# Kernel tuning notes

Measured on AMD Instinct MI355X. Metric: run time of the kernel, lower is better.

Reference implementation:

```python
import jax, jax.numpy as jnp
import numpy as np

N, E, D, DOUT = 2048, 1024, 64, 64


def setup_inputs() -> dict:
    key = jax.random.key(0)
    ks = jax.random.split(key, 8)
    x = jax.random.normal(ks[0], (N, D), dtype=jnp.float32)
    H = (jax.random.uniform(ks[1], (N, E)) < 0.05).astype(jnp.float32)
    s1 = 1.0 / np.sqrt(2 * D)
    W1 = jax.random.uniform(ks[2], (2 * D, 2 * D), jnp.float32, -s1, s1)  # att_proj1 [out=2D, in=2D]
    b1 = jax.random.uniform(ks[3], (2 * D,), jnp.float32, -s1, s1)
    W2 = jax.random.uniform(ks[4], (1, 2 * D), jnp.float32, -s1, s1)      # att_proj2 [1, 2D]
    b2 = jax.random.uniform(ks[5], (1,), jnp.float32, -s1, s1)
    sl = 1.0 / np.sqrt(D)
    Wl = jax.random.uniform(ks[6], (DOUT, D), jnp.float32, -sl, sl)       # linear [out, in]
    bl = jax.random.uniform(ks[7], (DOUT,), jnp.float32, -sl, sl)
    return dict(x=x, H=H, W1=W1, b1=b1, W2=W2, b2=b2, Wl=Wl, bl=bl)


def reference(x, H, W1, b1, W2, b2, Wl, bl):
    # edge features = sum of member node features: H.T @ x -> [E, D]
    ef = H.T @ x
    # att_proj1(concat(node, edge)) split into the two weight halves; the
    # concat itself never needs materializing, only the relu hidden [N, E, 2D].
    node_part = x @ W1[:, :D].T            # [N, 2D]
    edge_part = ef @ W1[:, D:].T           # [E, 2D]
    hidden = jax.nn.relu(node_part[:, None, :] + edge_part[None, :, :] + b1)  # [N, E, 2D]
    score = jnp.einsum('neh,h->ne', hidden, W2[0]) + b2[0]                    # [N, E]
    H_att = jax.nn.sigmoid(score) * H
    # symmetric degree normalization; diag-matmuls are elementwise scalings
    deg_n = jnp.sum(H, axis=1)             # [N]
    deg_e = jnp.sum(H, axis=0)             # [E]
    dn = jnp.where(deg_n > 0, deg_n ** -0.5, 0.0)   # nan_to_num(deg^-0.5)
    de = jnp.where(deg_e > 0, 1.0 / deg_e, 0.0)     # nan_to_num(deg^-1)
    y = dn[:, None] * (H_att @ (de[:, None] * (H_att.T @ (dn[:, None] * x))))
    return y @ Wl.T + bl
```

## Files before the change

### kernel.cpp

```cpp
#include <hip/hip_runtime.h>
#include <math.h>

#define NN 2048
#define EE 1024

typedef unsigned long long ull;
typedef unsigned short ushortt;

__global__ __launch_bounds__(512)
void k_scan(const float* __restrict__ H, const float* __restrict__ x,
            const float* __restrict__ W1, const float* __restrict__ b1,
            ushortt* __restrict__ elist, int* __restrict__ cnt,
            float* __restrict__ dn,
            ushortt* __restrict__ clist, int* __restrict__ ccnt,
            float* __restrict__ de,
            float* __restrict__ npb) {
  __shared__ __align__(16) float smem[64 * 129 + 8 * 64];
  __shared__ ushortt cbuf[8][4][64];
  __shared__ int csh[8][4];
  int bid = blockIdx.x, t = threadIdx.x, wv = t >> 6, lane = t & 63;
  ull below = (1ull << lane) - 1ull;
  if (bid < 256) {
    int e0 = bid * 4;
    int cs[4] = {0, 0, 0, 0};
    #pragma unroll
    for (int it = 0; it < 4; ++it) {
      int r = wv * 256 + it * 64 + lane;
      float4 hv = *(const float4*)&H[(size_t)r * EE + e0];
      float va[4] = {hv.x, hv.y, hv.z, hv.w};
      #pragma unroll
      for (int col = 0; col < 4; ++col) {
        ull m = __ballot(va[col] != 0.f);
        int pos = cs[col] + __popcll(m & below);
        if (va[col] != 0.f && pos < 64) cbuf[wv][col][pos] = (ushortt)r;
        cs[col] += __popcll(m);
      }
    }
    if (lane == 0) {
      #pragma unroll
      for (int col = 0; col < 4; ++col) csh[wv][col] = cs[col];
    }
    __syncthreads();
    if (wv < 4) {
      int col = wv, e = e0 + col;
      int base = 0, total = 0;
      #pragma unroll
      for (int u = 0; u < 8; ++u) {
        int cu = csh[u][col];
        int cc = min(cu, 64);
        for (int i = lane; i < cc; i += 64) {
          int p = base + i;
          if (p < 192) clist[e * 192 + p] = cbuf[u][col][i];
        }
        base += cc;
        total += cu;
      }
      if (lane == 0) {
        ccnt[e] = total;
        de[e] = total ? 1.f / (float)total : 0.f;
      }
    }
  } else if (bid < 512) {
    int n = (bid - 256) * 8 + wv;
    const float* row = H + (size_t)n * EE;
    int count = 0;
    #pragma unroll
    for (int it = 0; it < 4; ++it) {
      float4 hv = *(const float4*)&row[it * 256 + lane * 4];
      float va[4] = {hv.x, hv.y, hv.z, hv.w};
      ull m[4];
      #pragma unroll
      for (int c2 = 0; c2 < 4; ++c2) m[c2] = __ballot(va[c2] != 0.f);
      int rl = 0;
      #pragma unroll
      for (int c2 = 0; c2 < 4; ++c2) rl += __popcll(m[c2] & below);
      int within = 0;
      #pragma unroll
      for (int c2 = 0; c2 < 4; ++c2) {
        if (va[c2] != 0.f) {
          int pos = count + rl + within;
          if (pos < 128) elist[n * 128 + pos] = (ushortt)(it * 256 + lane * 4 + c2);
          ++within;
        }
      }
      #pragma unroll
      for (int c2 = 0; c2 < 4; ++c2) count += __popcll(m[c2]);
    }
    if (lane == 0) {
      cnt[n] = count;
      dn[n] = count ? rsqrtf((float)count) : 0.f;
    }
  } else {
    float* Wt = smem;
    float* xl = smem + 64 * 129;
    int r0 = (bid - 512) * 8;
    #pragma unroll
    for (int p = 0; p < 16; ++p) {
      int j = t + p * 512;
      int h = j >> 6, d = j & 63;
      Wt[d * 129 + h] = W1[h * 128 + d];
    }
    {
      int r = t >> 6, d = t & 63;
      xl[r * 64 + d] = x[(size_t)(r0 + r) * 64 + d];
    }
    __syncthreads();
    #pragma unroll
    for (int k = 0; k < 2; ++k) {
      int idx = t + k * 512;
      int row = idx >> 7, h = idx & 127;
      float acc = b1[h];
      #pragma unroll 8
      for (int d = 0; d < 64; ++d)
        acc += xl[row * 64 + d] * Wt[d * 129 + h];
      npb[(size_t)(r0 + row) * 128 + h] = acc;
    }
  }
}

__global__ __launch_bounds__(512)
void k_edge(const ushortt* __restrict__ clist,
            const int* __restrict__ ccnt, const float* __restrict__ de,
            const float* __restrict__ dn, const float* __restrict__ x,
            const float* __restrict__ W1, const float* __restrict__ npb,
            const float* __restrict__ W2, const float* __restrict__ b2,
            float* __restrict__ svc, float* __restrict__ w) {
  __shared__ __align__(16) float Wt[64 * 129];
  __shared__ __align__(16) float psum[8][64];
  __shared__ __align__(16) float efl[64];
  __shared__ __align__(16) float epl[128];
  __shared__ __align__(16) float pp[4][128];
  __shared__ __align__(16) float w2l[128];
  __shared__ __align__(16) float sval[192];
  __shared__ __align__(16) ushortt cls[192];
  int t = threadIdx.x, wv = t >> 6, lane = t & 63;
  int e = blockIdx.x;
  int c = min(ccnt[e], 192);
  #pragma unroll
  for (int p = 0; p < 16; ++p) {
    int j = t + p * 512;
    int h = j >> 6, d = j & 63;
    Wt[d * 129 + h] = W1[h * 128 + 64 + d];
  }
  if (t < 128) w2l[t] = W2[t];
  if (t < 96) ((uint*)cls)[t] = ((const uint*)(clist + (size_t)e * 192))[t];
  __syncthreads();
  float xv[24];
  {
    float a0 = 0.f, a1 = 0.f, a2 = 0.f, a3 = 0.f;
    #pragma unroll
    for (int k = 0; k < 24; ++k) {
      int j = wv + k * 8;
      float v = 0.f;
      if (j < c) v = x[(size_t)cls[j] * 64 + lane];
      xv[k] = v;
      if ((k & 3) == 0) a0 += v;
      else if ((k & 3) == 1) a1 += v;
      else if ((k & 3) == 2) a2 += v;
      else a3 += v;
    }
    psum[wv][lane] = (a0 + a1) + (a2 + a3);
  }
  __syncthreads();
  if (wv == 0) {
    float s = 0.f;
    #pragma unroll
    for (int u = 0; u < 8; ++u) s += psum[u][lane];
    efl[lane] = s;
  }
  __syncthreads();
  {
    int h = t & 127, q = t >> 7;
    float a = 0.f;
    #pragma unroll
    for (int d = q * 16; d < q * 16 + 16; ++d)
      a += efl[d] * Wt[d * 129 + h];
    pp[q][h] = a;
  }
  __syncthreads();
  if (t < 128) epl[t] = pp[0][t] + pp[1][t] + pp[2][t] + pp[3][t];
  __syncthreads();
  {
    int sub = t & 3, jloc = t >> 2;
    float b2v = b2[0];
    int nb = (c + 127) >> 7;
    for (int b = 0; b < nb; ++b) {
      int j = b * 128 + jloc;
      if (j < c) {
        int n = cls[j];
        const float* npr = npb + (size_t)n * 128;
        float a = 0.f;
        #pragma unroll
        for (int q = 0; q < 8; ++q) {
          int o = q * 16 + sub * 4;
          float4 av = *(const float4*)&npr[o];
          float4 ev = *(const float4*)&epl[o];
          float4 w2 = *(const float4*)&w2l[o];
          a += fmaxf(av.x + ev.x, 0.f) * w2.x + fmaxf(av.y + ev.y, 0.f) * w2.y
             + fmaxf(av.z + ev.z, 0.f) * w2.z + fmaxf(av.w + ev.w, 0.f) * w2.w;
        }
        a += __shfl_xor(a, 1, 64);
        a += __shfl_xor(a, 2, 64);
        if (sub == 0) {
          float sg = 1.f / (1.f + __expf(-(a + b2v)));
          sval[j] = dn[n] * sg;
          svc[(size_t)e * 192 + j] = sg;
        }
      }
    }
  }
  __syncthreads();
  {
    float a0 = 0.f, a1 = 0.f, a2 = 0.f, a3 = 0.f;
    #pragma unroll
    for (int k = 0; k < 24; ++k) {
      int j = wv + k * 8;
      float v = 0.f;
      if (j < c) v = sval[j] * xv[k];
      if ((k & 3) == 0) a0 += v;
      else if ((k & 3) == 1) a1 += v;
      else if ((k & 3) == 2) a2 += v;
      else a3 += v;
    }
    psum[wv][lane] = (a0 + a1) + (a2 + a3);
  }
  __syncthreads();
  if (wv == 0) {
    float s = 0.f;
    #pragma unroll
    for (int u = 0; u < 8; ++u) s += psum[u][lane];
    w[(size_t)e * 64 + lane] = de[e] * s;
  }
}

__global__ __launch_bounds__(512)
void k_node(const ushortt* __restrict__ elist, const int* __restrict__ cnt,
            const float* __restrict__ dn,
            const ushortt* __restrict__ clist, const int* __restrict__ ccnt,
            const float* __restrict__ svc, const float* __restrict__ w,
            const float* __restrict__ Wlg, const float* __restrict__ bl,
            float* __restrict__ out) {
  __shared__ __align__(16) float Wlds[64 * 65];
  __shared__ __align__(16) float sval[2][128];
  __shared__ __align__(16) float psum[8][64];
  __shared__ __align__(16) float zl[2][64];
  __shared__ __align__(16) ushortt els[2][128];
  int t = threadIdx.x, wv = t >> 6, lane = t & 63;
  int n0 = blockIdx.x * 2;
  #pragma unroll
  for (int p = 0; p < 8; ++p) {
    int j = t + p * 512;
    Wlds[(j >> 6) * 65 + (j & 63)] = Wlg[j];
  }
  if (t < 128) ((uint*)els)[t] = ((const uint*)(elist + (size_t)n0 * 128))[t];
  __syncthreads();
  if (t < 256) {
    int nd = t >> 7, jj = t & 127;
    int n = n0 + nd;
    int c = min(cnt[n], 128);
    if (jj < c) {
      int e = els[nd][jj];
      const ushortt* cl = clist + (size_t)e * 192;
      int lo = 0, hi = min(ccnt[e], 192);
      while (lo < hi) {
        int mid = (lo + hi) >> 1;
        if (cl[mid] < n) lo = mid + 1; else hi = mid;
      }
      sval[nd][jj] = svc[(size_t)e * 192 + lo];
    }
  }
  __syncthreads();
  {
    int nd = wv >> 2;
    int n = n0 + nd;
    int c = min(cnt[n], 128);
    float a0 = 0.f, a1 = 0.f, a2 = 0.f, a3 = 0.f;
    #pragma unroll
    for (int k = 0; k < 32; ++k) {
      int j = (wv & 3) + k * 4;
      float v = 0.f;
      if (j < c) v = sval[nd][j] * w[(size_t)els[nd][j] * 64 + lane];
      if ((k & 3) == 0) a0 += v;
      else if ((k & 3) == 1) a1 += v;
      else if ((k & 3) == 2) a2 += v;
      else a3 += v;
    }
    psum[wv][lane] = (a0 + a1) + (a2 + a3);
    __syncthreads();
    if ((wv & 3) == 0)
      zl[nd][lane] = dn[n] * (psum[wv][lane] + psum[wv + 1][lane] +
                              psum[wv + 2][lane] + psum[wv + 3][lane]);
  }
  __syncthreads();
  {
    float* pp = (float*)psum;
    int o = t & 63, nd = (t >> 6) & 1, q = t >> 7;
    float po = 0.f;
    #pragma unroll
    for (int d = q * 16; d < q * 16 + 16; ++d)
      po += zl[nd][d] * Wlds[o * 65 + d];
    pp[q * 128 + nd * 64 + o] = po;
    __syncthreads();
    if (t < 128) {
      int ndo = t >> 6, oo = t & 63;
      out[(size_t)(n0 + ndo) * 64 + oo] =
          bl[oo] + pp[0 * 128 + t] + pp[1 * 128 + t] + pp[2 * 128 + t] + pp[3 * 128 + t];
    }
  }
}

extern "C" void kernel_launch(void* const* d_in, const int* in_sizes, int n_in,
                              void* d_out, int out_size, void* d_ws, size_t ws_size,
                              hipStream_t stream) {
  const float* x  = (const float*)d_in[0];
  const float* H  = (const float*)d_in[1];
  const float* W1 = (const float*)d_in[2];
  const float* b1 = (const float*)d_in[3];
  const float* W2 = (const float*)d_in[4];
  const float* b2 = (const float*)d_in[5];
  const float* Wl = (const float*)d_in[6];
  const float* bl = (const float*)d_in[7];
  float* out = (float*)d_out;

  char* wsb = (char*)d_ws;
  float* dn   = (float*)wsb;  wsb += NN * 4;
  float* de   = (float*)wsb;  wsb += EE * 4;
  int*   cnt  = (int*)wsb;    wsb += NN * 4;
  int*   ccnt = (int*)wsb;    wsb += EE * 4;
  float* npb  = (float*)wsb;  wsb += (size_t)NN * 128 * 4;
  float* w    = (float*)wsb;  wsb += (size_t)EE * 64 * 4;
  float* svc  = (float*)wsb;  wsb += (size_t)EE * 192 * 4;
  ushortt* elist = (ushortt*)wsb; wsb += (size_t)NN * 128 * 2;
  ushortt* clist = (ushortt*)wsb; wsb += (size_t)EE * 192 * 2;

  hipLaunchKernelGGL(k_scan, dim3(768), dim3(512), 0, stream,
                     H, x, W1, b1, elist, cnt, dn, clist, ccnt, de, npb);
  hipLaunchKernelGGL(k_edge, dim3(EE), dim3(512), 0, stream,
                     clist, ccnt, de, dn, x, W1, npb, W2, b2, svc, w);
  hipLaunchKernelGGL(k_node, dim3(NN / 2), dim3(512), 0, stream,
                     elist, cnt, dn, clist, ccnt, svc, w, Wl, bl, out);
}
```

Before: 40.90 us.

## Store sigmoid scores in dense edge-by-node table and drop LDS weight transpose

The edge kernel now writes each sigmoid score into a dense [E, N] table indexed by node id, so the node kernel reads it directly instead of binary-searching the edge's member list. The edge kernel also stops staging the transposed W1 half in shared memory and reads W1 rows from global memory with float4 loads. It re-reads x in the second pass instead of keeping a 24-element register array. The fixed unrolled loops become loops bounded by the actual count, which cuts LDS use and register pressure at the cost of an 8 MB sparsely written workspace and repeated global reads.

```diff
diff --git a/kernel.cpp b/kernel.cpp
--- a/kernel.cpp
+++ b/kernel.cpp
@@ -124,8 +124,7 @@
             const float* __restrict__ dn, const float* __restrict__ x,
             const float* __restrict__ W1, const float* __restrict__ npb,
             const float* __restrict__ W2, const float* __restrict__ b2,
-            float* __restrict__ svc, float* __restrict__ w) {
-  __shared__ __align__(16) float Wt[64 * 129];
+            float* __restrict__ sigc, float* __restrict__ w) {
   __shared__ __align__(16) float psum[8][64];
   __shared__ __align__(16) float efl[64];
   __shared__ __align__(16) float epl[128];
@@ -136,28 +135,23 @@
   int t = threadIdx.x, wv = t >> 6, lane = t & 63;
   int e = blockIdx.x;
   int c = min(ccnt[e], 192);
-  #pragma unroll
-  for (int p = 0; p < 16; ++p) {
-    int j = t + p * 512;
-    int h = j >> 6, d = j & 63;
-    Wt[d * 129 + h] = W1[h * 128 + 64 + d];
-  }
   if (t < 128) w2l[t] = W2[t];
   if (t < 96) ((uint*)cls)[t] = ((const uint*)(clist + (size_t)e * 192))[t];
   __syncthreads();
-  float xv[24];
   {
     float a0 = 0.f, a1 = 0.f, a2 = 0.f, a3 = 0.f;
-    #pragma unroll
-    for (int k = 0; k < 24; ++k) {
-      int j = wv + k * 8;
-      float v = 0.f;
-      if (j < c) v = x[(size_t)cls[j] * 64 + lane];
-      xv[k] = v;
-      if ((k & 3) == 0) a0 += v;
-      else if ((k & 3) == 1) a1 += v;
-      else if ((k & 3) == 2) a2 += v;
-      else a3 += v;
+    for (int j = wv; j < c; j += 64) {
+      #pragma unroll
+      for (int k = 0; k < 8; ++k) {
+        int jj = j + k * 8;
+        if (jj < c) {
+          float v = x[(size_t)cls[jj] * 64 + lane];
+          if ((k & 3) == 0) a0 += v;
+          else if ((k & 3) == 1) a1 += v;
+          else if ((k & 3) == 2) a2 += v;
+          else a3 += v;
+        }
+      }
     }
     psum[wv][lane] = (a0 + a1) + (a2 + a3);
   }
@@ -171,10 +165,16 @@
   __syncthreads();
   {
     int h = t & 127, q = t >> 7;
-    float a = 0.f;
-    #pragma unroll
-    for (int d = q * 16; d < q * 16 + 16; ++d)
-      a += efl[d] * Wt[d * 129 + h];
+    const float* wr = W1 + h * 128 + 64 + q * 16;
+    float4 w0 = *(const float4*)&wr[0];
+    float4 w1 = *(const float4*)&wr[4];
+    float4 w2 = *(const float4*)&wr[8];
+    float4 w3 = *(const float4*)&wr[12];
+    const float* ef = efl + q * 16;
+    float a = ef[0] * w0.x + ef[1] * w0.y + ef[2] * w0.z + ef[3] * w0.w
+            + ef[4] * w1.x + ef[5] * w1.y + ef[6] * w1.z + ef[7] * w1.w
+            + ef[8] * w2.x + ef[9] * w2.y + ef[10] * w2.z + ef[11] * w2.w
+            + ef[12] * w3.x + ef[13] * w3.y + ef[14] * w3.z + ef[15] * w3.w;
     pp[q][h] = a;
   }
   __syncthreads();
@@ -204,7 +204,7 @@
         if (sub == 0) {
           float sg = 1.f / (1.f + __expf(-(a + b2v)));
           sval[j] = dn[n] * sg;
-          svc[(size_t)e * 192 + j] = sg;
+          sigc[(size_t)e * NN + n] = sg;
         }
       }
     }
@@ -212,15 +212,18 @@
   __syncthreads();
   {
     float a0 = 0.f, a1 = 0.f, a2 = 0.f, a3 = 0.f;
-    #pragma unroll
-    for (int k = 0; k < 24; ++k) {
-      int j = wv + k * 8;
-      float v = 0.f;
-      if (j < c) v = sval[j] * xv[k];
-      if ((k & 3) == 0) a0 += v;
-      else if ((k & 3) == 1) a1 += v;
-      else if ((k & 3) == 2) a2 += v;
-      else a3 += v;
+    for (int j = wv; j < c; j += 64) {
+      #pragma unroll
+      for (int k = 0; k < 8; ++k) {
+        int jj = j + k * 8;
+        if (jj < c) {
+          float v = sval[jj] * x[(size_t)cls[jj] * 64 + lane];
+          if ((k & 3) == 0) a0 += v;
+          else if ((k & 3) == 1) a1 += v;
+          else if ((k & 3) == 2) a2 += v;
+          else a3 += v;
+        }
+      }
     }
     psum[wv][lane] = (a0 + a1) + (a2 + a3);
   }
@@ -235,9 +238,8 @@
 
 __global__ __launch_bounds__(512)
 void k_node(const ushortt* __restrict__ elist, const int* __restrict__ cnt,
-            const float* __restrict__ dn,
-            const ushortt* __restrict__ clist, const int* __restrict__ ccnt,
-            const float* __restrict__ svc, const float* __restrict__ w,
+            const float* __restrict__ dn, const float* __restrict__ sigc,
+            const float* __restrict__ w,
             const float* __restrict__ Wlg, const float* __restrict__ bl,
             float* __restrict__ out) {
   __shared__ __align__(16) float Wlds[64 * 65];
@@ -260,13 +262,7 @@
     int c = min(cnt[n], 128);
     if (jj < c) {
       int e = els[nd][jj];
-      const ushortt* cl = clist + (size_t)e * 192;
-      int lo = 0, hi = min(ccnt[e], 192);
-      while (lo < hi) {
-        int mid = (lo + hi) >> 1;
-        if (cl[mid] < n) lo = mid + 1; else hi = mid;
-      }
-      sval[nd][jj] = svc[(size_t)e * 192 + lo];
+      sval[nd][jj] = sigc[(size_t)e * NN + n];
     }
   }
   __syncthreads();
@@ -275,15 +271,18 @@
     int n = n0 + nd;
     int c = min(cnt[n], 128);
     float a0 = 0.f, a1 = 0.f, a2 = 0.f, a3 = 0.f;
-    #pragma unroll
-    for (int k = 0; k < 32; ++k) {
-      int j = (wv & 3) + k * 4;
-      float v = 0.f;
-      if (j < c) v = sval[nd][j] * w[(size_t)els[nd][j] * 64 + lane];
-      if ((k & 3) == 0) a0 += v;
-      else if ((k & 3) == 1) a1 += v;
-      else if ((k & 3) == 2) a2 += v;
-      else a3 += v;
+    for (int j = wv & 3; j < c; j += 32) {
+      #pragma unroll
+      for (int k = 0; k < 8; ++k) {
+        int jj = j + k * 4;
+        if (jj < c) {
+          float v = sval[nd][jj] * w[(size_t)els[nd][jj] * 64 + lane];
+          if ((k & 3) == 0) a0 += v;
+          else if ((k & 3) == 1) a1 += v;
+          else if ((k & 3) == 2) a2 += v;
+          else a3 += v;
+        }
+      }
     }
     psum[wv][lane] = (a0 + a1) + (a2 + a3);
     __syncthreads();
@@ -329,14 +328,14 @@
   int*   ccnt = (int*)wsb;    wsb += EE * 4;
   float* npb  = (float*)wsb;  wsb += (size_t)NN * 128 * 4;
   float* w    = (float*)wsb;  wsb += (size_t)EE * 64 * 4;
-  float* svc  = (float*)wsb;  wsb += (size_t)EE * 192 * 4;
+  float* sigc = (float*)wsb;  wsb += (size_t)EE * NN * 4;
   ushortt* elist = (ushortt*)wsb; wsb += (size_t)NN * 128 * 2;
   ushortt* clist = (ushortt*)wsb; wsb += (size_t)EE * 192 * 2;
 
   hipLaunchKernelGGL(k_scan, dim3(768), dim3(512), 0, stream,
                      H, x, W1, b1, elist, cnt, dn, clist, ccnt, de, npb);
   hipLaunchKernelGGL(k_edge, dim3(EE), dim3(512), 0, stream,
-                     clist, ccnt, de, dn, x, W1, npb, W2, b2, svc, w);
+                     clist, ccnt, de, dn, x, W1, npb, W2, b2, sigc, w);
   hipLaunchKernelGGL(k_node, dim3(NN / 2), dim3(512), 0, stream,
-                     elist, cnt, dn, clist, ccnt, svc, w, Wl, bl, out);
+                     elist, cnt, dn, sigc, w, Wl, bl, out);
 }
```

Result: slower. 49.99 us (+22.2%).
